# Performance work log

Measured on AMD Instinct MI355X. Metric: run time of the kernel, lower is better.

The kernel has to match this reference:

```python
import jax, jax.numpy as jnp
import numpy as np

B, E, H, NE, K, P, IMG, NC, FF, DEPTH = 64, 256, 8, 4, 2, 16, 224, 38, 1024, 4
S = (IMG // P) ** 2 + 1  # 197 tokens (cls + patches)


def layernorm(x, w, b, eps=1e-5):
    m = x.mean(-1, keepdims=True)
    v = ((x - m) ** 2).mean(-1, keepdims=True)
    return (x - m) / jnp.sqrt(v + eps) * w + b


def forward(x, conv_w, conv_b, cls_token, pos_embed, ln1_w, ln1_b, qkv_w, qkv_b,
            out_w, out_b, ln2_w, ln2_b, router_w, router_b, e_w1, e_b1, e_w2, e_b2,
            norm_w, norm_b, h1_w, h1_b, h2_w, h2_b):
    Bn = x.shape[0]
    dh = E // H
    # patch embedding: conv stride=kernel=P
    z = jax.lax.conv_general_dilated(x, conv_w, (P, P), 'VALID',
                                     dimension_numbers=('NCHW', 'OIHW', 'NCHW'))
    z = z + conv_b[None, :, None, None]
    z = z.reshape(Bn, E, -1).transpose(0, 2, 1)  # [B, 196, E]
    z = jnp.concatenate([jnp.broadcast_to(cls_token, (Bn, 1, E)), z], axis=1) + pos_embed
    for i in range(DEPTH):
        # --- multi-head self-attention ---
        h = layernorm(z, ln1_w[i], ln1_b[i])
        qkv = h @ qkv_w[i] + qkv_b[i]                       # [B,S,3E]
        q, k, v = jnp.split(qkv, 3, axis=-1)
        q = q.reshape(Bn, -1, H, dh)
        k = k.reshape(Bn, -1, H, dh)
        v = v.reshape(Bn, -1, H, dh)
        att = jax.nn.softmax(jnp.einsum('bqhd,bkhd->bhqk', q, k) / jnp.sqrt(jnp.float32(dh)), axis=-1)
        ctx = jnp.einsum('bhqk,bkhd->bqhd', att, v).reshape(Bn, -1, E)
        z = z + ctx @ out_w[i] + out_b[i]
        # --- MoE FFN (top-k routing; expert sum expressed densely via gate weights) ---
        xf = layernorm(z, ln2_w[i], ln2_b[i]).reshape(-1, E)  # [T,E]
        probs = jax.nn.softmax(xf @ router_w[i] + router_b[i], axis=-1)  # [T,NE]
        wk, idx = jax.lax.top_k(probs, K)
        wk = wk / wk.sum(-1, keepdims=True)
        gate = (jax.nn.one_hot(idx, NE, dtype=wk.dtype) * wk[..., None]).sum(1)  # [T,NE]
        he = jax.nn.gelu(jnp.einsum('td,ndh->tnh', xf, e_w1[i]) + e_b1[i], approximate=False)
        oe = jnp.einsum('tnh,nhd->tnd', he, e_w2[i]) + e_b2[i]
        z = z + jnp.einsum('tnd,tn->td', oe, gate).reshape(Bn, -1, E)
    cls = layernorm(z[:, 0], norm_w, norm_b)
    h = jax.nn.gelu(cls @ h1_w + h1_b, approximate=False)
    return h @ h2_w + h2_b  # [B, NC]


def setup_inputs() -> dict:
    key = jax.random.key(0)
    ks = jax.random.split(key, 12)
    s = jnp.float32(0.02)
    return {
        'x': jax.random.normal(ks[0], (B, 3, IMG, IMG), jnp.float32),
        'conv_w': jax.random.normal(ks[1], (E, 3, P, P), jnp.float32) * s,
        'conv_b': jnp.zeros((E,), jnp.float32),
        'cls_token': jax.random.normal(ks[2], (1, 1, E), jnp.float32) * s,
        'pos_embed': jax.random.normal(ks[3], (1, S, E), jnp.float32) * s,
        'ln1_w': jnp.ones((DEPTH, E), jnp.float32), 'ln1_b': jnp.zeros((DEPTH, E), jnp.float32),
        'qkv_w': jax.random.normal(ks[4], (DEPTH, E, 3 * E), jnp.float32) * s,
        'qkv_b': jnp.zeros((DEPTH, 3 * E), jnp.float32),
        'out_w': jax.random.normal(ks[5], (DEPTH, E, E), jnp.float32) * s,
        'out_b': jnp.zeros((DEPTH, E), jnp.float32),
        'ln2_w': jnp.ones((DEPTH, E), jnp.float32), 'ln2_b': jnp.zeros((DEPTH, E), jnp.float32),
        'router_w': jax.random.normal(ks[6], (DEPTH, E, NE), jnp.float32) * s,
        'router_b': jnp.zeros((DEPTH, NE), jnp.float32),
        'e_w1': jax.random.normal(ks[7], (DEPTH, NE, E, FF), jnp.float32) * s,
        'e_b1': jnp.zeros((DEPTH, NE, FF), jnp.float32),
        'e_w2': jax.random.normal(ks[8], (DEPTH, NE, FF, E), jnp.float32) * s,
        'e_b2': jnp.zeros((DEPTH, NE, E), jnp.float32),
        'norm_w': jnp.ones((E,), jnp.float32), 'norm_b': jnp.zeros((E,), jnp.float32),
        'h1_w': jax.random.normal(ks[9], (E, E), jnp.float32) * s,
        'h1_b': jnp.zeros((E,), jnp.float32),
        'h2_w': jax.random.normal(ks[10], (E, NC), jnp.float32) * s,
        'h2_b': jnp.zeros((NC,), jnp.float32),
    }


def reference(x, conv_w, conv_b, cls_token, pos_embed, ln1_w, ln1_b, qkv_w, qkv_b,
              out_w, out_b, ln2_w, ln2_b, router_w, router_b, e_w1, e_b1, e_w2, e_b2,
              norm_w, norm_b, h1_w, h1_b, h2_w, h2_b):
    return forward(x, conv_w, conv_b, cls_token, pos_embed, ln1_w, ln1_b, qkv_w, qkv_b,
                   out_w, out_b, ln2_w, ln2_b, router_w, router_b, e_w1, e_b1, e_w2, e_b2,
                   norm_w, norm_b, h1_w, h1_b, h2_w, h2_b)
```

## Files before the change

kernel.cpp:

```cpp
#include <hip/hip_runtime.h>
#include <hip/hip_bf16.h>

#define T_TOK 12608
#define MPAD  12672
#define S_TOK 197
#define DEPTH_L 4

typedef __attribute__((ext_vector_type(8))) short short8;
typedef __attribute__((ext_vector_type(4))) short short4v;
typedef __attribute__((ext_vector_type(4))) float f32x4;

using gvoid = __attribute__((address_space(1))) const void;
using lvoid = __attribute__((address_space(3))) void;

__device__ __forceinline__ float gelu_f(float x) {
    return 0.5f * x * (1.f + erff(x * 0.70710678118654752440f));
}

__device__ __forceinline__ void split2(float v, __hip_bfloat16& h, __hip_bfloat16& l) {
    h = __float2bfloat16(v);
    l = __float2bfloat16(v - __bfloat162float(h));
}

__device__ __forceinline__ int base_of(const int* __restrict__ cnt, int e) {
    int b = 0;
#pragma unroll
    for (int k = 0; k < 3; ++k) if (e > k) b += cnt[k];
    return b;
}

template<int MODE>
__global__ __launch_bounds__(256, 4)
void gemm3(const short* __restrict__ Ahi, const short* __restrict__ Alo, int ldA,
           const short* __restrict__ Bext,
           float* __restrict__ outf, __hip_bfloat16* __restrict__ outh, int ldOut,
           const float* __restrict__ bias, const float* __restrict__ gate,
           const float* __restrict__ aux,
           const int* __restrict__ rowmap, const int* __restrict__ cntp,
           int Mvalid, int N, int K, int npanels, int kChunk, size_t outStride)
{
    __shared__ short As[128 * 64];
    __shared__ short Bs[128 * 64];
    const int tid  = threadIdx.x;
    const int wid  = tid >> 6;
    const int lane = tid & 63;

    const int xcd = blockIdx.x & 7;
    const int j   = blockIdx.x >> 3;
    const int p   = (j % 13) * 8 + xcd;
    const int c   = j / 13;
    if (p >= npanels) return;
    const int row0 = p * 128;
    const int col0 = c * 128;

    const int wr = (wid >> 1) * 64;
    const int wc = (wid & 1) * 64;
    const int e  = (MODE == 2 || MODE == 3) ? blockIdx.z : 0;

    int Mv = Mvalid;
    int baseRow = 0;
    const int* rmap = nullptr;
    if (MODE == 2 || MODE == 3) {
        Mv = cntp[e];
        if (row0 >= Mv) return;
        baseRow = base_of(cntp, e);
        if (MODE == 2) rmap = rowmap + e * T_TOK;
    }

    int arow[4];
    if (MODE == 2) {
#pragma unroll
        for (int i = 0; i < 4; ++i) {
            int gr = row0 + (i * 4 + wid) * 8 + (lane >> 3);
            if (gr > Mv - 1) gr = Mv - 1;
            arow[i] = rmap[gr];
        }
    }

    f32x4 acc[4][4];
#pragma unroll
    for (int m = 0; m < 4; ++m)
#pragma unroll
        for (int n = 0; n < 4; ++n) acc[m][n] = (f32x4){0.f, 0.f, 0.f, 0.f};

    const int ld3 = 3 * K;
    const size_t strideA = (size_t)ldA * 2;
    const size_t strideB = (size_t)ld3 * 2;
    const char* Bbase = (const char*)Bext + ((size_t)e * N + col0) * strideB;

    const int kBeg = blockIdx.y * kChunk;
    int kEnd = kBeg + kChunk; if (kEnd > ld3) kEnd = ld3;

    for (int k0 = kBeg; k0 < kEnd; k0 += 64) {
        const int regio = (k0 >= K) + (k0 >= 2 * K);
        const short* Asrc = (regio == 1) ? Alo : Ahi;
        const int ka = k0 - regio * K;
        __syncthreads();
#pragma unroll
        for (int i = 0; i < 4; ++i) {
            const int chunk = (i * 4 + wid) * 1024;
            const int off = chunk + lane * 16;
            const int r = off >> 7;
            const int cb = off & 127;
            const int cbs = cb ^ ((r & 7) << 4);
            const char* asrc;
            if (MODE == 2) {
                asrc = (const char*)Asrc + (size_t)arow[i] * strideA + (size_t)ka * 2 + cbs;
            } else {
                asrc = (const char*)Asrc + (size_t)(baseRow + row0 + r) * strideA + (size_t)ka * 2 + cbs;
            }
            __builtin_amdgcn_global_load_lds((gvoid*)asrc, (lvoid*)((char*)As + chunk), 16, 0, 0);
            __builtin_amdgcn_global_load_lds(
                (gvoid*)(Bbase + (size_t)r * strideB + (size_t)k0 * 2 + cbs),
                (lvoid*)((char*)Bs + chunk), 16, 0, 0);
        }
        __syncthreads();

        const int lr = lane & 15;
        const int kbB = (lane >> 4) * 16;
#pragma unroll
        for (int kk = 0; kk < 2; ++kk) {
            short8 af[4], bfr[4];
#pragma unroll
            for (int m = 0; m < 4; ++m) {
                const int row = wr + m * 16 + lr;
                const int cbb = (kk * 64 + kbB) ^ ((row & 7) << 4);
                af[m] = *(const short8*)((const char*)As + row * 128 + cbb);
            }
#pragma unroll
            for (int n = 0; n < 4; ++n) {
                const int row = wc + n * 16 + lr;
                const int cbb = (kk * 64 + kbB) ^ ((row & 7) << 4);
                bfr[n] = *(const short8*)((const char*)Bs + row * 128 + cbb);
            }
#pragma unroll
            for (int m = 0; m < 4; ++m)
#pragma unroll
                for (int n = 0; n < 4; ++n)
                    acc[m][n] = __builtin_amdgcn_mfma_f32_16x16x32_bf16(af[m], bfr[n], acc[m][n], 0, 0, 0);
        }
    }

    const int lr = lane & 15;
    const int rb4 = (lane >> 4) * 4;
#pragma unroll
    for (int m = 0; m < 4; ++m) {
#pragma unroll
        for (int n = 0; n < 4; ++n) {
#pragma unroll
            for (int r = 0; r < 4; ++r) {
                const int row = row0 + wr + m * 16 + rb4 + r;
                const int col = col0 + wc + n * 16 + lr;
                if (row >= Mv) continue;
                const float v = acc[m][n][r];
                if (MODE == 0) {
                    outf[(size_t)row * N + col] = v + bias[col];
                } else if (MODE == 1) {
                    outf[(size_t)row * N + col] += v + bias[col];
                } else if (MODE == 2) {
                    const float g = gate[rmap[row] * 4 + e];
                    const float y = g * gelu_f(v + bias[e * N + col]);
                    __hip_bfloat16 h, l; split2(y, h, l);
                    outh[((size_t)(baseRow + row)) * ldOut + col] = h;
                    outh[((size_t)(baseRow + row)) * ldOut + N + col] = l;
                } else if (MODE == 3) {
                    outf[outStride * blockIdx.y + ((size_t)(baseRow + row)) * N + col] = v;
                } else if (MODE == 4) {
                    const int bi = row / 196;
                    const int pp = row - bi * 196;
                    outf[((size_t)(bi * 197 + 1 + pp)) * N + col] = v + bias[col] + aux[(size_t)(1 + pp) * N + col];
                }
            }
        }
    }
}

__global__ void ln_split(const float* __restrict__ x, const float* __restrict__ w,
                         const float* __restrict__ b, __hip_bfloat16* __restrict__ hi,
                         __hip_bfloat16* __restrict__ lo, float* __restrict__ out32,
                         int nrows, int in_stride)
{
    const int row = blockIdx.x * 4 + (threadIdx.x >> 6);
    const int lane = threadIdx.x & 63;
    if (row >= nrows) return;
    const float4 v = ((const float4*)(x + (size_t)row * in_stride))[lane];
    float s = v.x + v.y + v.z + v.w;
#pragma unroll
    for (int o = 32; o; o >>= 1) s += __shfl_xor(s, o);
    const float mean = s * (1.f / 256.f);
    const float dx = v.x - mean, dy = v.y - mean, dz = v.z - mean, dw = v.w - mean;
    float q = dx * dx + dy * dy + dz * dz + dw * dw;
#pragma unroll
    for (int o = 32; o; o >>= 1) q += __shfl_xor(q, o);
    const float inv = rsqrtf(q * (1.f / 256.f) + 1e-5f);
    const int c = lane * 4;
    const float4 wv = ((const float4*)w)[lane];
    const float4 bv = ((const float4*)b)[lane];
    float y[4];
    y[0] = dx * inv * wv.x + bv.x;
    y[1] = dy * inv * wv.y + bv.y;
    y[2] = dz * inv * wv.z + bv.z;
    y[3] = dw * inv * wv.w + bv.w;
    if (hi) {
#pragma unroll
        for (int j = 0; j < 4; ++j) {
            __hip_bfloat16 h, l; split2(y[j], h, l);
            hi[(size_t)row * 256 + c + j] = h;
            lo[(size_t)row * 256 + c + j] = l;
        }
    }
    if (out32) {
        ((float4*)(out32 + (size_t)row * 256))[lane] = make_float4(y[0], y[1], y[2], y[3]);
    }
}

__global__ void ln2_router(const float* __restrict__ x, const float* __restrict__ w,
                           const float* __restrict__ b, __hip_bfloat16* __restrict__ hi,
                           __hip_bfloat16* __restrict__ lo,
                           const float* __restrict__ rw, const float* __restrict__ rb,
                           float* __restrict__ gate, int* __restrict__ top2,
                           int* __restrict__ cnt, int T)
{
    if (blockIdx.x == 0 && threadIdx.x < 4) cnt[threadIdx.x] = 0;
    const int row = blockIdx.x * 4 + (threadIdx.x >> 6);
    const int lane = threadIdx.x & 63;
    if (row >= T) return;
    const float4 v = ((const float4*)(x + (size_t)row * 256))[lane];
    float s = v.x + v.y + v.z + v.w;
#pragma unroll
    for (int o = 32; o; o >>= 1) s += __shfl_xor(s, o);
    const float mean = s * (1.f / 256.f);
    const float dx = v.x - mean, dy = v.y - mean, dz = v.z - mean, dw = v.w - mean;
    float q = dx * dx + dy * dy + dz * dz + dw * dw;
#pragma unroll
    for (int o = 32; o; o >>= 1) q += __shfl_xor(q, o);
    const float inv = rsqrtf(q * (1.f / 256.f) + 1e-5f);
    const int c = lane * 4;
    const float4 wv = ((const float4*)w)[lane];
    const float4 bv = ((const float4*)b)[lane];
    float y[4];
    y[0] = dx * inv * wv.x + bv.x;
    y[1] = dy * inv * wv.y + bv.y;
    y[2] = dz * inv * wv.z + bv.z;
    y[3] = dw * inv * wv.w + bv.w;
#pragma unroll
    for (int jj = 0; jj < 4; ++jj) {
        __hip_bfloat16 h, l; split2(y[jj], h, l);
        hi[(size_t)row * 256 + c + jj] = h;
        lo[(size_t)row * 256 + c + jj] = l;
    }
    float a0 = 0, a1 = 0, a2 = 0, a3 = 0;
#pragma unroll
    for (int jj = 0; jj < 4; ++jj) {
        const float xs = y[jj];
        const float4 wr4 = ((const float4*)rw)[lane * 4 + jj];
        a0 += xs * wr4.x; a1 += xs * wr4.y; a2 += xs * wr4.z; a3 += xs * wr4.w;
    }
#pragma unroll
    for (int o = 32; o; o >>= 1) {
        a0 += __shfl_xor(a0, o); a1 += __shfl_xor(a1, o);
        a2 += __shfl_xor(a2, o); a3 += __shfl_xor(a3, o);
    }
    if (lane == 0) {
        float l[4] = {a0 + rb[0], a1 + rb[1], a2 + rb[2], a3 + rb[3]};
        const float m = fmaxf(fmaxf(l[0], l[1]), fmaxf(l[2], l[3]));
        float pr[4]; float sm = 0.f;
#pragma unroll
        for (int n = 0; n < 4; ++n) { pr[n] = expf(l[n] - m); sm += pr[n]; }
#pragma unroll
        for (int n = 0; n < 4; ++n) pr[n] /= sm;
        int i0 = 0;
        for (int n = 1; n < 4; ++n) if (pr[n] > pr[i0]) i0 = n;
        int i1 = -1;
        for (int n = 0; n < 4; ++n) { if (n == i0) continue; if (i1 < 0 || pr[n] > pr[i1]) i1 = n; }
        const float wsum = pr[i0] + pr[i1];
        float g[4] = {0.f, 0.f, 0.f, 0.f};
        g[i0] = pr[i0] / wsum; g[i1] = pr[i1] / wsum;
        ((float4*)gate)[row] = make_float4(g[0], g[1], g[2], g[3]);
        top2[row] = i0 | (i1 << 4);
    }
}

__global__ void build_list(const int* __restrict__ top2, int* __restrict__ cnt,
                           int* __restrict__ list, int* __restrict__ poslist, int T)
{
    const int t = blockIdx.x * 256 + threadIdx.x;
    const int lane = threadIdx.x & 63;
    int i0 = -1, i1 = -1;
    if (t < T) { const int v = top2[t]; i0 = v & 15; i1 = v >> 4; }
    const unsigned long long lt = (lane == 63) ? ~0ull >> 1 : (1ull << lane) - 1;
#pragma unroll
    for (int e = 0; e < 4; ++e) {
#pragma unroll
        for (int s = 0; s < 2; ++s) {
            const int sel = s ? i1 : i0;
            const unsigned long long m = __ballot(sel == e);
            if (m) {
                const int leader = __ffsll((long long)m) - 1;
                int base = 0;
                if (lane == leader) base = atomicAdd(&cnt[e], __popcll(m));
                base = __shfl(base, leader);
                if (sel == e) {
                    const int p = base + __popcll(m & lt);
                    list[e * T_TOK + p] = t;
                    poslist[2 * t + s] = p;
                }
            }
        }
    }
}

__global__ void combine_ln(const float* __restrict__ ebuf, size_t sliceOff,
                           const int* __restrict__ top2,
                           const int* __restrict__ poslist, const int* __restrict__ cnt,
                           const float* __restrict__ gate, const float* __restrict__ e_b2,
                           float* __restrict__ z,
                           const float* __restrict__ lnw, const float* __restrict__ lnb,
                           __hip_bfloat16* __restrict__ hi, __hip_bfloat16* __restrict__ lo,
                           int T)
{
    const int t = blockIdx.x * 4 + (threadIdx.x >> 6);
    const int lane = threadIdx.x & 63;
    if (t >= T) return;
    const int tp = top2[t];
    const int e0 = tp & 15, e1 = tp >> 4;
    const size_t g0 = (size_t)base_of(cnt, e0) + poslist[2 * t];
    const size_t g1 = (size_t)base_of(cnt, e1) + poslist[2 * t + 1];
    const float4 a  = ((const float4*)(ebuf + g0 * 256))[lane];
    const float4 bq = ((const float4*)(ebuf + g1 * 256))[lane];
    const float4 a2 = ((const float4*)(ebuf + sliceOff + g0 * 256))[lane];
    const float4 b2q = ((const float4*)(ebuf + sliceOff + g1 * 256))[lane];
    const float4 gw = ((const float4*)gate)[t];
    const float4 b0 = ((const float4*)(e_b2 + 0 * 256))[lane];
    const float4 b1 = ((const float4*)(e_b2 + 1 * 256))[lane];
    const float4 b2 = ((const float4*)(e_b2 + 2 * 256))[lane];
    const float4 b3 = ((const float4*)(e_b2 + 3 * 256))[lane];
    float4* zp = (float4*)(z + (size_t)t * 256);
    float4 acc = zp[lane];
    acc.x += (a.x + a2.x) + (bq.x + b2q.x) + gw.x * b0.x + gw.y * b1.x + gw.z * b2.x + gw.w * b3.x;
    acc.y += (a.y + a2.y) + (bq.y + b2q.y) + gw.x * b0.y + gw.y * b1.y + gw.z * b2.y + gw.w * b3.y;
    acc.z += (a.z + a2.z) + (bq.z + b2q.z) + gw.x * b0.z + gw.y * b1.z + gw.z * b2.z + gw.w * b3.z;
    acc.w += (a.w + a2.w) + (bq.w + b2q.w) + gw.x * b0.w + gw.y * b1.w + gw.z * b2.w + gw.w * b3.w;
    zp[lane] = acc;
    if (lnw) {
        float s = acc.x + acc.y + acc.z + acc.w;
#pragma unroll
        for (int o = 32; o; o >>= 1) s += __shfl_xor(s, o);
        const float mean = s * (1.f / 256.f);
        const float dx = acc.x - mean, dy = acc.y - mean, dz = acc.z - mean, dw = acc.w - mean;
        float q = dx * dx + dy * dy + dz * dz + dw * dw;
#pragma unroll
        for (int o = 32; o; o >>= 1) q += __shfl_xor(q, o);
        const float inv = rsqrtf(q * (1.f / 256.f) + 1e-5f);
        const int c = lane * 4;
        const float4 wv = ((const float4*)lnw)[lane];
        const float4 bv = ((const float4*)lnb)[lane];
        float y[4];
        y[0] = dx * inv * wv.x + bv.x;
        y[1] = dy * inv * wv.y + bv.y;
        y[2] = dz * inv * wv.z + bv.z;
        y[3] = dw * inv * wv.w + bv.w;
#pragma unroll
        for (int jj = 0; jj < 4; ++jj) {
            __hip_bfloat16 h, l; split2(y[jj], h, l);
            hi[(size_t)t * 256 + c + jj] = h;
            lo[(size_t)t * 256 + c + jj] = l;
        }
    }
}

#define VSTR 232
__global__ __launch_bounds__(256, 1)
void attn_v6(const float* __restrict__ qkv, __hip_bfloat16* __restrict__ ctxhi,
             __hip_bfloat16* __restrict__ ctxlo)
{
    __shared__ short Qhf[13 * 512], Qlf[13 * 512], Khf[13 * 512], Klf[13 * 512];
    __shared__ short Vth[32 * VSTR], Vtl[32 * VSTR];
    __shared__ short Pfh[4 * 512], Pfl[4 * 512];
    const int b = blockIdx.x >> 3;
    const int h = blockIdx.x & 7;
    const int tid = threadIdx.x, lane = tid & 63, wid = tid >> 6;
    const int g = lane >> 4;
    const size_t base = ((size_t)b * S_TOK) * 768 + h * 32;

    for (int idx = tid; idx < 208 * 8; idx += 256) {
        const int s = idx >> 3, c4 = idx & 7;
        float4 qv = make_float4(0.f, 0.f, 0.f, 0.f);
        float4 kv = make_float4(0.f, 0.f, 0.f, 0.f);
        if (s < S_TOK) {
            const float* row = qkv + base + (size_t)s * 768;
            qv = *(const float4*)(row + c4 * 4);
            kv = *(const float4*)(row + 256 + c4 * 4);
        }
        short4v qh, ql, kh, kl;
#pragma unroll
        for (int j = 0; j < 4; ++j) {
            __hip_bfloat16 hh, ll;
            split2((&qv.x)[j], hh, ll);
            qh[j] = *reinterpret_cast<short*>(&hh); ql[j] = *reinterpret_cast<short*>(&ll);
            split2((&kv.x)[j], hh, ll);
            kh[j] = *reinterpret_cast<short*>(&hh); kl[j] = *reinterpret_cast<short*>(&ll);
        }
        const int off = (s >> 4) * 512 + ((s & 15) + ((c4 >> 1) << 4)) * 8 + (c4 & 1) * 4;
        *(short4v*)&Qhf[off] = qh; *(short4v*)&Qlf[off] = ql;
        *(short4v*)&Khf[off] = kh; *(short4v*)&Klf[off] = kl;
    }
    for (int idx = tid; idx < S_TOK * 8; idx += 256) {
        const int s = idx >> 3, c4 = idx & 7;
        const float4 vv = *(const float4*)(qkv + base + (size_t)s * 768 + 512 + c4 * 4);
#pragma unroll
        for (int j = 0; j < 4; ++j) {
            __hip_bfloat16 hh, ll; split2((&vv.x)[j], hh, ll);
            Vth[(c4 * 4 + j) * VSTR + s] = *reinterpret_cast<short*>(&hh);
            Vtl[(c4 * 4 + j) * VSTR + s] = *reinterpret_cast<short*>(&ll);
        }
    }
    for (int idx = tid; idx < 32 * (VSTR - S_TOK); idx += 256) {
        const int d = idx / (VSTR - S_TOK), s = S_TOK + idx % (VSTR - S_TOK);
        Vth[d * VSTR + s] = 0;
        Vtl[d * VSTR + s] = 0;
    }
    __syncthreads();

    const float scale = 0.17677669529663687f;
    for (int qt = wid; qt < 13; qt += 4) {
        const short8 qh  = *(const short8*)&Qhf[qt * 512 + lane * 8];
        const short8 qlo = *(const short8*)&Qlf[qt * 512 + lane * 8];
        f32x4 o0 = (f32x4){0.f, 0.f, 0.f, 0.f};
        f32x4 o1 = (f32x4){0.f, 0.f, 0.f, 0.f};
        float lsum = 0.f;
        for (int kp = 0; kp < 7; ++kp) {
#pragma unroll
            for (int half = 0; half < 2; ++half) {
                const int kt = kp * 2 + half;
                short4v pkh = (short4v){0, 0, 0, 0};
                short4v pkl = (short4v){0, 0, 0, 0};
                if (kt < 13) {
                    const short8 kh = *(const short8*)&Khf[kt * 512 + lane * 8];
                    const short8 kl = *(const short8*)&Klf[kt * 512 + lane * 8];
                    f32x4 st = (f32x4){0.f, 0.f, 0.f, 0.f};
                    st = __builtin_amdgcn_mfma_f32_16x16x32_bf16(kh, qh,  st, 0, 0, 0);
                    st = __builtin_amdgcn_mfma_f32_16x16x32_bf16(kl, qh,  st, 0, 0, 0);
                    st = __builtin_amdgcn_mfma_f32_16x16x32_bf16(kh, qlo, st, 0, 0, 0);
#pragma unroll
                    for (int r = 0; r < 4; ++r) {
                        const int sg = kt * 16 + g * 4 + r;
                        const float e = (sg < S_TOK) ? __expf(st[r] * scale) : 0.f;
                        lsum += e;
                        __hip_bfloat16 hh, ll; split2(e, hh, ll);
                        pkh[r] = *reinterpret_cast<short*>(&hh);
                        pkl[r] = *reinterpret_cast<short*>(&ll);
                    }
                }
                const int slb = half * 16 + g * 4;
                const int lp = (lane & 15) + ((slb >> 3) << 4);
                *(short4v*)&Pfh[wid * 512 + lp * 8 + (slb & 4)] = pkh;
                *(short4v*)&Pfl[wid * 512 + lp * 8 + (slb & 4)] = pkl;
            }
            asm volatile("s_waitcnt lgkmcnt(0)" ::: "memory");
            __builtin_amdgcn_sched_barrier(0);
            const short8 pfh = *(const short8*)&Pfh[wid * 512 + lane * 8];
            const short8 pfl = *(const short8*)&Pfl[wid * 512 + lane * 8];
            const int vo = kp * 32 + g * 8;
            const short8 vah = *(const short8*)&Vth[(lane & 15) * VSTR + vo];
            const short8 valo = *(const short8*)&Vtl[(lane & 15) * VSTR + vo];
            const short8 vbh = *(const short8*)&Vth[((lane & 15) + 16) * VSTR + vo];
            const short8 vblo = *(const short8*)&Vtl[((lane & 15) + 16) * VSTR + vo];
            o0 = __builtin_amdgcn_mfma_f32_16x16x32_bf16(vah,  pfh, o0, 0, 0, 0);
            o0 = __builtin_amdgcn_mfma_f32_16x16x32_bf16(vah,  pfl, o0, 0, 0, 0);
            o0 = __builtin_amdgcn_mfma_f32_16x16x32_bf16(valo, pfh, o0, 0, 0, 0);
            o1 = __builtin_amdgcn_mfma_f32_16x16x32_bf16(vbh,  pfh, o1, 0, 0, 0);
            o1 = __builtin_amdgcn_mfma_f32_16x16x32_bf16(vbh,  pfl, o1, 0, 0, 0);
            o1 = __builtin_amdgcn_mfma_f32_16x16x32_bf16(vblo, pfh, o1, 0, 0, 0);
        }
        float lr = lsum;
        lr += __shfl_xor(lr, 16);
        lr += __shfl_xor(lr, 32);
        const int q = qt * 16 + (lane & 15);
        if (q < S_TOK) {
            const float inv = 1.f / lr;
            const size_t orow = ((size_t)b * S_TOK + q) * 256 + h * 32;
#pragma unroll
            for (int r = 0; r < 4; ++r) {
                __hip_bfloat16 hh, ll;
                split2(o0[r] * inv, hh, ll);
                ctxhi[orow + g * 4 + r] = hh;
                ctxlo[orow + g * 4 + r] = ll;
                split2(o1[r] * inv, hh, ll);
                ctxhi[orow + 16 + g * 4 + r] = hh;
                ctxlo[orow + 16 + g * 4 + r] = ll;
            }
        }
    }
}

__global__ void transpose_split(const float* __restrict__ in, short* __restrict__ out,
                                int K, int N, size_t inBatch, size_t outBatch)
{
    __shared__ float tile[32][33];
    const int n0 = blockIdx.x * 32, k0 = blockIdx.y * 32;
    const float* src = in + blockIdx.z * inBatch;
    __hip_bfloat16* dst = (__hip_bfloat16*)out + blockIdx.z * outBatch;
    const int tx = threadIdx.x & 31, ty = threadIdx.x >> 5;
#pragma unroll
    for (int i = 0; i < 32; i += 8)
        tile[ty + i][tx] = src[(size_t)(k0 + ty + i) * N + (n0 + tx)];
    __syncthreads();
    const int ld3 = 3 * K;
#pragma unroll
    for (int i = 0; i < 32; i += 8) {
        const float v = tile[tx][ty + i];
        __hip_bfloat16 h, l; split2(v, h, l);
        const int n = n0 + ty + i, k = k0 + tx;
        dst[(size_t)n * ld3 + k] = h;
        dst[(size_t)n * ld3 + K + k] = h;
        dst[(size_t)n * ld3 + 2 * K + k] = l;
    }
}

__global__ void split_rows(const float* __restrict__ in, short* __restrict__ out, int N, int K)
{
    const int idx = blockIdx.x * 256 + threadIdx.x;
    if (idx >= N * K) return;
    const int n = idx / K, k = idx - n * K;
    __hip_bfloat16 h, l; split2(in[idx], h, l);
    __hip_bfloat16* dst = (__hip_bfloat16*)out;
    dst[(size_t)n * 3 * K + k] = h;
    dst[(size_t)n * 3 * K + K + k] = h;
    dst[(size_t)n * 3 * K + 2 * K + k] = l;
}

__global__ void im2col_split(const float* __restrict__ x, short* __restrict__ out)
{
    const int t = blockIdx.x;
    const int b = t / 196, p = t - b * 196;
    const int py = p / 14, px = p - py * 14;
    __hip_bfloat16* dst = (__hip_bfloat16*)out;
    for (int c_ = threadIdx.x; c_ < 768; c_ += 256) {
        const int c = c_ >> 8, r = c_ & 255;
        const int ky = r >> 4, kx = r & 15;
        const float v = x[(((size_t)b * 3 + c) * 224 + (py * 16 + ky)) * 224 + (px * 16 + kx)];
        __hip_bfloat16 h, l; split2(v, h, l);
        dst[(size_t)t * 1536 + c_] = h;
        dst[(size_t)t * 1536 + 768 + c_] = l;
    }
}

__global__ void cls_init(const float* __restrict__ cls_tok, const float* __restrict__ pos,
                         float* __restrict__ z)
{
    const int b = blockIdx.x, e = threadIdx.x;
    z[((size_t)b * S_TOK) * 256 + e] = cls_tok[e] + pos[e];
}

__global__ void head1_kernel(const float* __restrict__ clsln, const float* __restrict__ w,
                             const float* __restrict__ bias, float* __restrict__ hbuf)
{
    __shared__ float xs[256];
    const int b = blockIdx.x, n = threadIdx.x;
    xs[n] = clsln[b * 256 + n];
    __syncthreads();
    float acc = bias[n];
    for (int k = 0; k < 256; ++k) acc += xs[k] * w[k * 256 + n];
    hbuf[b * 256 + n] = gelu_f(acc);
}

__global__ void head2_kernel(const float* __restrict__ hbuf, const float* __restrict__ w,
                             const float* __restrict__ bias, float* __restrict__ out)
{
    __shared__ float xs[256];
    const int b = blockIdx.x, t = threadIdx.x;
    xs[t] = hbuf[b * 256 + t];
    __syncthreads();
    if (t < 38) {
        float acc = bias[t];
        for (int k = 0; k < 256; ++k) acc += xs[k] * w[k * 38 + t];
        out[b * 38 + t] = acc;
    }
}

extern "C" void kernel_launch(void* const* d_in, const int* in_sizes, int n_in,
                              void* d_out, int out_size, void* d_ws, size_t ws_size,
                              hipStream_t stream)
{
    const float* x       = (const float*)d_in[0];
    const float* conv_w  = (const float*)d_in[1];
    const float* conv_b  = (const float*)d_in[2];
    const float* cls_tok = (const float*)d_in[3];
    const float* pos     = (const float*)d_in[4];
    const float* ln1_w   = (const float*)d_in[5];
    const float* ln1_b   = (const float*)d_in[6];
    const float* qkv_w   = (const float*)d_in[7];
    const float* qkv_b   = (const float*)d_in[8];
    const float* out_w   = (const float*)d_in[9];
    const float* out_b   = (const float*)d_in[10];
    const float* ln2_w   = (const float*)d_in[11];
    const float* ln2_b   = (const float*)d_in[12];
    const float* rw      = (const float*)d_in[13];
    const float* rb      = (const float*)d_in[14];
    const float* e_w1    = (const float*)d_in[15];
    const float* e_b1    = (const float*)d_in[16];
    const float* e_w2    = (const float*)d_in[17];
    const float* e_b2    = (const float*)d_in[18];
    const float* norm_w  = (const float*)d_in[19];
    const float* norm_b  = (const float*)d_in[20];
    const float* h1_w    = (const float*)d_in[21];
    const float* h1_b    = (const float*)d_in[22];
    const float* h2_w    = (const float*)d_in[23];
    const float* h2_b    = (const float*)d_in[24];
    float* outp = (float*)d_out;

    char* ws = (char*)d_ws;
    size_t off = 0;
    auto alloc = [&](size_t bytes) -> char* {
        char* p = ws + off;
        off += (bytes + 255) & ~(size_t)255;
        return p;
    };

    float* zbuf    = (float*)alloc((size_t)T_TOK * 256 * 4);
    short* xfhi    = (short*)alloc((size_t)MPAD * 256 * 2);
    short* xflo    = (short*)alloc((size_t)MPAD * 256 * 2);
    float* qkvbuf  = (float*)alloc((size_t)T_TOK * 768 * 4);
    float* ebuf    = qkvbuf;
    float* ebuf1   = (float*)alloc((size_t)(2 * T_TOK) * 256 * 4);
    short* ctxhi   = (short*)alloc((size_t)MPAD * 256 * 2);
    short* ctxlo   = (short*)alloc((size_t)MPAD * 256 * 2);
    float* gate    = (float*)alloc((size_t)T_TOK * 4 * 4);
    short* he_full = (short*)alloc((size_t)(2 * MPAD) * 2048 * 2);
    short* patches = he_full;
    short* qkvWall = (short*)alloc((size_t)DEPTH_L * 768 * 768 * 2);
    short* woutAll = (short*)alloc((size_t)DEPTH_L * 256 * 768 * 2);
    short* w1All   = (short*)alloc((size_t)DEPTH_L * 4 * 1024 * 768 * 2);
    short* w2All   = (short*)alloc((size_t)DEPTH_L * 4 * 256 * 3072 * 2);
    short* convext = (short*)alloc((size_t)256 * 2304 * 2);
    float* clsln   = (float*)alloc((size_t)64 * 256 * 4);
    float* hbuf    = (float*)alloc((size_t)64 * 256 * 4);
    int*   elist   = (int*)alloc((size_t)4 * T_TOK * 4);
    int*   poslist = (int*)alloc((size_t)2 * T_TOK * 4);
    int*   ecnt    = (int*)alloc(256);
    int*   top2    = (int*)alloc((size_t)T_TOK * 4);

    const size_t sliceOff = (size_t)(ebuf1 - ebuf);

    transpose_split<<<dim3(24, 8, DEPTH_L), 256, 0, stream>>>(qkv_w, qkvWall,
                                                              256, 768, 196608, 589824);
    transpose_split<<<dim3(8, 8, DEPTH_L), 256, 0, stream>>>(out_w, woutAll,
                                                             256, 256, 65536, 196608);
    transpose_split<<<dim3(32, 8, 4 * DEPTH_L), 256, 0, stream>>>(e_w1, w1All,
                                                                  256, 1024, 262144, 786432);
    transpose_split<<<dim3(8, 32, 4 * DEPTH_L), 256, 0, stream>>>(e_w2, w2All,
                                                                  1024, 256, 262144, 786432);
    split_rows<<<768, 256, 0, stream>>>(conv_w, convext, 256, 768);

    im2col_split<<<12544, 256, 0, stream>>>(x, patches);
    gemm3<4><<<208, 256, 0, stream>>>(patches, patches + 768, 1536, convext,
                                      zbuf, nullptr, 0, conv_b, nullptr, pos,
                                      nullptr, nullptr, 12544, 256, 768, 98,
                                      3 * 768, 0);
    cls_init<<<64, 256, 0, stream>>>(cls_tok, pos, zbuf);

    ln_split<<<3152, 256, 0, stream>>>(zbuf, ln1_w, ln1_b,
                                       (__hip_bfloat16*)xfhi, (__hip_bfloat16*)xflo,
                                       nullptr, T_TOK, 256);

    for (int i = 0; i < DEPTH_L; ++i) {
        gemm3<0><<<624, 256, 0, stream>>>(xfhi, xflo, 256, qkvWall + (size_t)i * 589824,
                                          qkvbuf, nullptr, 0, qkv_b + i * 768,
                                          nullptr, nullptr, nullptr, nullptr,
                                          T_TOK, 768, 256, 99, 3 * 256, 0);
        attn_v6<<<512, 256, 0, stream>>>(qkvbuf, (__hip_bfloat16*)ctxhi, (__hip_bfloat16*)ctxlo);
        gemm3<1><<<208, 256, 0, stream>>>(ctxhi, ctxlo, 256, woutAll + (size_t)i * 196608,
                                          zbuf, nullptr, 0, out_b + i * 256,
                                          nullptr, nullptr, nullptr, nullptr,
                                          T_TOK, 256, 256, 99, 3 * 256, 0);
        ln2_router<<<3152, 256, 0, stream>>>(zbuf, ln2_w + i * 256, ln2_b + i * 256,
                                             (__hip_bfloat16*)xfhi, (__hip_bfloat16*)xflo,
                                             rw + i * 1024, rb + i * 4, gate, top2, ecnt, T_TOK);
        build_list<<<50, 256, 0, stream>>>(top2, ecnt, elist, poslist, T_TOK);
        gemm3<2><<<dim3(832, 1, 4), 256, 0, stream>>>(xfhi, xflo, 256,
                                                      w1All + (size_t)i * 4 * 786432,
                                                      nullptr, (__hip_bfloat16*)he_full, 2048,
                                                      e_b1 + (size_t)i * 4096, gate, nullptr,
                                                      elist, ecnt, T_TOK, 1024, 256, 99,
                                                      3 * 256, 0);
        gemm3<3><<<dim3(208, 2, 4), 256, 0, stream>>>(he_full, he_full + 1024, 2048,
                                                      w2All + (size_t)i * 4 * 786432,
                                                      ebuf, nullptr, 0, nullptr, nullptr, nullptr,
                                                      nullptr, ecnt, T_TOK, 256, 1024, 99,
                                                      1536, sliceOff);
        if (i < DEPTH_L - 1) {
            combine_ln<<<3152, 256, 0, stream>>>(ebuf, sliceOff, top2, poslist, ecnt, gate,
                                                 e_b2 + (size_t)i * 1024, zbuf,
                                                 ln1_w + (i + 1) * 256, ln1_b + (i + 1) * 256,
                                                 (__hip_bfloat16*)xfhi, (__hip_bfloat16*)xflo,
                                                 T_TOK);
        } else {
            combine_ln<<<3152, 256, 0, stream>>>(ebuf, sliceOff, top2, poslist, ecnt, gate,
                                                 e_b2 + (size_t)i * 1024, zbuf,
                                                 nullptr, nullptr, nullptr, nullptr, T_TOK);
        }
    }

    ln_split<<<16, 256, 0, stream>>>(zbuf, norm_w, norm_b, nullptr, nullptr, clsln, 64, S_TOK * 256);
    head1_kernel<<<64, 256, 0, stream>>>(clsln, h1_w, h1_b, hbuf);
    head2_kernel<<<64, 256, 0, stream>>>(hbuf, h2_w, h2_b, outp);

    (void)in_sizes; (void)n_in; (void)out_size; (void)ws_size;
}
```

Before: 1.369 ms.

## Reuse A_hi tile for both B_hi and B_lo in split-bf16 GEMM

The three-pass split-bf16 GEMM (Ahi*Bhi + Alo*Bhi + Ahi*Blo) previously streamed a 3K-long extended K dimension, loading Ahi twice and storing Bhi twice. Now each K step loads Ahi once with both Bhi and Blo tiles into two LDS buffers, computes both products, then loads Alo and reuses the Bhi tile. This cuts global A and B traffic by about a third and shrinks the pre-split weight buffers to 2K. In exchange LDS use per block rises from 32KB to 48KB, and each iteration gets an extra pair of barriers.

```diff
diff --git a/kernel.cpp b/kernel.cpp
--- a/kernel.cpp
+++ b/kernel.cpp
@@ -40,7 +40,8 @@
            int Mvalid, int N, int K, int npanels, int kChunk, size_t outStride)
 {
     __shared__ short As[128 * 64];
-    __shared__ short Bs[128 * 64];
+    __shared__ short Bs0[128 * 64];
+    __shared__ short Bs1[128 * 64];
     const int tid  = threadIdx.x;
     const int wid  = tid >> 6;
     const int lane = tid & 63;
@@ -83,18 +84,18 @@
 #pragma unroll
         for (int n = 0; n < 4; ++n) acc[m][n] = (f32x4){0.f, 0.f, 0.f, 0.f};
 
-    const int ld3 = 3 * K;
+    const int ld2 = 2 * K;
     const size_t strideA = (size_t)ldA * 2;
-    const size_t strideB = (size_t)ld3 * 2;
+    const size_t strideB = (size_t)ld2 * 2;
     const char* Bbase = (const char*)Bext + ((size_t)e * N + col0) * strideB;
 
     const int kBeg = blockIdx.y * kChunk;
-    int kEnd = kBeg + kChunk; if (kEnd > ld3) kEnd = ld3;
+    int kEnd = kBeg + kChunk; if (kEnd > K) kEnd = K;
+
+    const int lr = lane & 15;
+    const int kbB = (lane >> 4) * 16;
 
     for (int k0 = kBeg; k0 < kEnd; k0 += 64) {
-        const int regio = (k0 >= K) + (k0 >= 2 * K);
-        const short* Asrc = (regio == 1) ? Alo : Ahi;
-        const int ka = k0 - regio * K;
         __syncthreads();
 #pragma unroll
         for (int i = 0; i < 4; ++i) {
@@ -105,19 +106,20 @@
             const int cbs = cb ^ ((r & 7) << 4);
             const char* asrc;
             if (MODE == 2) {
-                asrc = (const char*)Asrc + (size_t)arow[i] * strideA + (size_t)ka * 2 + cbs;
+                asrc = (const char*)Ahi + (size_t)arow[i] * strideA + (size_t)k0 * 2 + cbs;
             } else {
-                asrc = (const char*)Asrc + (size_t)(baseRow + row0 + r) * strideA + (size_t)ka * 2 + cbs;
+                asrc = (const char*)Ahi + (size_t)(baseRow + row0 + r) * strideA + (size_t)k0 * 2 + cbs;
             }
             __builtin_amdgcn_global_load_lds((gvoid*)asrc, (lvoid*)((char*)As + chunk), 16, 0, 0);
             __builtin_amdgcn_global_load_lds(
                 (gvoid*)(Bbase + (size_t)r * strideB + (size_t)k0 * 2 + cbs),
-                (lvoid*)((char*)Bs + chunk), 16, 0, 0);
+                (lvoid*)((char*)Bs0 + chunk), 16, 0, 0);
+            __builtin_amdgcn_global_load_lds(
+                (gvoid*)(Bbase + (size_t)r * strideB + (size_t)(K + k0) * 2 + cbs),
+                (lvoid*)((char*)Bs1 + chunk), 16, 0, 0);
         }
         __syncthreads();
 
-        const int lr = lane & 15;
-        const int kbB = (lane >> 4) * 16;
 #pragma unroll
         for (int kk = 0; kk < 2; ++kk) {
             short8 af[4], bfr[4];
@@ -131,7 +133,7 @@
             for (int n = 0; n < 4; ++n) {
                 const int row = wc + n * 16 + lr;
                 const int cbb = (kk * 64 + kbB) ^ ((row & 7) << 4);
-                bfr[n] = *(const short8*)((const char*)Bs + row * 128 + cbb);
+                bfr[n] = *(const short8*)((const char*)Bs0 + row * 128 + cbb);
             }
 #pragma unroll
             for (int m = 0; m < 4; ++m)
@@ -139,9 +141,69 @@
                 for (int n = 0; n < 4; ++n)
                     acc[m][n] = __builtin_amdgcn_mfma_f32_16x16x32_bf16(af[m], bfr[n], acc[m][n], 0, 0, 0);
         }
-    }
-
-    const int lr = lane & 15;
+#pragma unroll
+        for (int kk = 0; kk < 2; ++kk) {
+            short8 af[4], bfr[4];
+#pragma unroll
+            for (int m = 0; m < 4; ++m) {
+                const int row = wr + m * 16 + lr;
+                const int cbb = (kk * 64 + kbB) ^ ((row & 7) << 4);
+                af[m] = *(const short8*)((const char*)As + row * 128 + cbb);
+            }
+#pragma unroll
+            for (int n = 0; n < 4; ++n) {
+                const int row = wc + n * 16 + lr;
+                const int cbb = (kk * 64 + kbB) ^ ((row & 7) << 4);
+                bfr[n] = *(const short8*)((const char*)Bs1 + row * 128 + cbb);
+            }
+#pragma unroll
+            for (int m = 0; m < 4; ++m)
+#pragma unroll
+                for (int n = 0; n < 4; ++n)
+                    acc[m][n] = __builtin_amdgcn_mfma_f32_16x16x32_bf16(af[m], bfr[n], acc[m][n], 0, 0, 0);
+        }
+
+        __syncthreads();
+#pragma unroll
+        for (int i = 0; i < 4; ++i) {
+            const int chunk = (i * 4 + wid) * 1024;
+            const int off = chunk + lane * 16;
+            const int r = off >> 7;
+            const int cb = off & 127;
+            const int cbs = cb ^ ((r & 7) << 4);
+            const char* asrc;
+            if (MODE == 2) {
+                asrc = (const char*)Alo + (size_t)arow[i] * strideA + (size_t)k0 * 2 + cbs;
+            } else {
+                asrc = (const char*)Alo + (size_t)(baseRow + row0 + r) * strideA + (size_t)k0 * 2 + cbs;
+            }
+            __builtin_amdgcn_global_load_lds((gvoid*)asrc, (lvoid*)((char*)As + chunk), 16, 0, 0);
+        }
+        __syncthreads();
+
+#pragma unroll
+        for (int kk = 0; kk < 2; ++kk) {
+            short8 af[4], bfr[4];
+#pragma unroll
+            for (int m = 0; m < 4; ++m) {
+                const int row = wr + m * 16 + lr;
+                const int cbb = (kk * 64 + kbB) ^ ((row & 7) << 4);
+                af[m] = *(const short8*)((const char*)As + row * 128 + cbb);
+            }
+#pragma unroll
+            for (int n = 0; n < 4; ++n) {
+                const int row = wc + n * 16 + lr;
+                const int cbb = (kk * 64 + kbB) ^ ((row & 7) << 4);
+                bfr[n] = *(const short8*)((const char*)Bs0 + row * 128 + cbb);
+            }
+#pragma unroll
+            for (int m = 0; m < 4; ++m)
+#pragma unroll
+                for (int n = 0; n < 4; ++n)
+                    acc[m][n] = __builtin_amdgcn_mfma_f32_16x16x32_bf16(af[m], bfr[n], acc[m][n], 0, 0, 0);
+        }
+    }
+
     const int rb4 = (lane >> 4) * 4;
 #pragma unroll
     for (int m = 0; m < 4; ++m) {
@@ -506,15 +568,14 @@
     for (int i = 0; i < 32; i += 8)
         tile[ty + i][tx] = src[(size_t)(k0 + ty + i) * N + (n0 + tx)];
     __syncthreads();
-    const int ld3 = 3 * K;
+    const int ld2 = 2 * K;
 #pragma unroll
     for (int i = 0; i < 32; i += 8) {
         const float v = tile[tx][ty + i];
         __hip_bfloat16 h, l; split2(v, h, l);
         const int n = n0 + ty + i, k = k0 + tx;
-        dst[(size_t)n * ld3 + k] = h;
-        dst[(size_t)n * ld3 + K + k] = h;
-        dst[(size_t)n * ld3 + 2 * K + k] = l;
+        dst[(size_t)n * ld2 + k] = h;
+        dst[(size_t)n * ld2 + K + k] = l;
     }
 }
 
@@ -525,9 +586,8 @@
     const int n = idx / K, k = idx - n * K;
     __hip_bfloat16 h, l; split2(in[idx], h, l);
     __hip_bfloat16* dst = (__hip_bfloat16*)out;
-    dst[(size_t)n * 3 * K + k] = h;
-    dst[(size_t)n * 3 * K + K + k] = h;
-    dst[(size_t)n * 3 * K + 2 * K + k] = l;
+    dst[(size_t)n * 2 * K + k] = h;
+    dst[(size_t)n * 2 * K + K + k] = l;
 }
 
 __global__ void im2col_split(const float* __restrict__ x, short* __restrict__ out)
@@ -629,11 +689,11 @@
     float* gate    = (float*)alloc((size_t)T_TOK * 4 * 4);
     short* he_full = (short*)alloc((size_t)(2 * MPAD) * 2048 * 2);
     short* patches = he_full;
-    short* qkvWall = (short*)alloc((size_t)DEPTH_L * 768 * 768 * 2);
-    short* woutAll = (short*)alloc((size_t)DEPTH_L * 256 * 768 * 2);
-    short* w1All   = (short*)alloc((size_t)DEPTH_L * 4 * 1024 * 768 * 2);
-    short* w2All   = (short*)alloc((size_t)DEPTH_L * 4 * 256 * 3072 * 2);
-    short* convext = (short*)alloc((size_t)256 * 2304 * 2);
+    short* qkvWall = (short*)alloc((size_t)DEPTH_L * 768 * 512 * 2);
+    short* woutAll = (short*)alloc((size_t)DEPTH_L * 256 * 512 * 2);
+    short* w1All   = (short*)alloc((size_t)DEPTH_L * 4 * 1024 * 512 * 2);
+    short* w2All   = (short*)alloc((size_t)DEPTH_L * 4 * 256 * 2048 * 2);
+    short* convext = (short*)alloc((size_t)256 * 1536 * 2);
     float* clsln   = (float*)alloc((size_t)64 * 256 * 4);
     float* hbuf    = (float*)alloc((size_t)64 * 256 * 4);
     int*   elist   = (int*)alloc((size_t)4 * T_TOK * 4);
@@ -644,20 +704,20 @@
     const size_t sliceOff = (size_t)(ebuf1 - ebuf);
 
     transpose_split<<<dim3(24, 8, DEPTH_L), 256, 0, stream>>>(qkv_w, qkvWall,
-                                                              256, 768, 196608, 589824);
+                                                              256, 768, 196608, 393216);
     transpose_split<<<dim3(8, 8, DEPTH_L), 256, 0, stream>>>(out_w, woutAll,
-                                                             256, 256, 65536, 196608);
+                                                             256, 256, 65536, 131072);
     transpose_split<<<dim3(32, 8, 4 * DEPTH_L), 256, 0, stream>>>(e_w1, w1All,
-                                                                  256, 1024, 262144, 786432);
+                                                                  256, 1024, 262144, 524288);
     transpose_split<<<dim3(8, 32, 4 * DEPTH_L), 256, 0, stream>>>(e_w2, w2All,
-                                                                  1024, 256, 262144, 786432);
+                                                                  1024, 256, 262144, 524288);
     split_rows<<<768, 256, 0, stream>>>(conv_w, convext, 256, 768);
 
     im2col_split<<<12544, 256, 0, stream>>>(x, patches);
     gemm3<4><<<208, 256, 0, stream>>>(patches, patches + 768, 1536, convext,
                                       zbuf, nullptr, 0, conv_b, nullptr, pos,
                                       nullptr, nullptr, 12544, 256, 768, 98,
-                                      3 * 768, 0);
+                                      768, 0);
     cls_init<<<64, 256, 0, stream>>>(cls_tok, pos, zbuf);
 
     ln_split<<<3152, 256, 0, stream>>>(zbuf, ln1_w, ln1_b,
@@ -665,30 +725,30 @@
                                        nullptr, T_TOK, 256);
 
     for (int i = 0; i < DEPTH_L; ++i) {
-        gemm3<0><<<624, 256, 0, stream>>>(xfhi, xflo, 256, qkvWall + (size_t)i * 589824,
+        gemm3<0><<<624, 256, 0, stream>>>(xfhi, xflo, 256, qkvWall + (size_t)i * 393216,
                                           qkvbuf, nullptr, 0, qkv_b + i * 768,
                                           nullptr, nullptr, nullptr, nullptr,
-                                          T_TOK, 768, 256, 99, 3 * 256, 0);
+                                          T_TOK, 768, 256, 99, 256, 0);
         attn_v6<<<512, 256, 0, stream>>>(qkvbuf, (__hip_bfloat16*)ctxhi, (__hip_bfloat16*)ctxlo);
-        gemm3<1><<<208, 256, 0, stream>>>(ctxhi, ctxlo, 256, woutAll + (size_t)i * 196608,
+        gemm3<1><<<208, 256, 0, stream>>>(ctxhi, ctxlo, 256, woutAll + (size_t)i * 131072,
                                           zbuf, nullptr, 0, out_b + i * 256,
                                           nullptr, nullptr, nullptr, nullptr,
-                                          T_TOK, 256, 256, 99, 3 * 256, 0);
+                                          T_TOK, 256, 256, 99, 256, 0);
         ln2_router<<<3152, 256, 0, stream>>>(zbuf, ln2_w + i * 256, ln2_b + i * 256,
                                              (__hip_bfloat16*)xfhi, (__hip_bfloat16*)xflo,
                                              rw + i * 1024, rb + i * 4, gate, top2, ecnt, T_TOK);
         build_list<<<50, 256, 0, stream>>>(top2, ecnt, elist, poslist, T_TOK);
         gemm3<2><<<dim3(832, 1, 4), 256, 0, stream>>>(xfhi, xflo, 256,
-                                                      w1All + (size_t)i * 4 * 786432,
+                                                      w1All + (size_t)i * 4 * 524288,
                                                       nullptr, (__hip_bfloat16*)he_full, 2048,
                                                       e_b1 + (size_t)i * 4096, gate, nullptr,
                                                       elist, ecnt, T_TOK, 1024, 256, 99,
-                                                      3 * 256, 0);
+                                                      256, 0);
         gemm3<3><<<dim3(208, 2, 4), 256, 0, stream>>>(he_full, he_full + 1024, 2048,
-                                                      w2All + (size_t)i * 4 * 786432,
+                                                      w2All + (size_t)i * 4 * 524288,
                                                       ebuf, nullptr, 0, nullptr, nullptr, nullptr,
                                                       nullptr, ecnt, T_TOK, 256, 1024, 99,
-                                                      1536, sliceOff);
+                                                      512, sliceOff);
         if (i < DEPTH_L - 1) {
             combine_ln<<<3152, 256, 0, stream>>>(ebuf, sliceOff, top2, poslist, ecnt, gate,
                                                  e_b2 + (size_t)i * 1024, zbuf,
```

Measured after the change: 1.462 ms. 1.07x slower.
